# Optimization experiments

Measured on AMD Instinct MI355X. Metric: run time of the kernel, lower is better.

The kernel has to match this reference:

```python
import jax, jax.numpy as jnp
import numpy as np

B, T, C = 2, 2048, 1024
H, D = 16, 64


def setup_inputs() -> dict:
    key = jax.random.key(0)
    ks = jax.random.split(key, 5)
    s = 1.0 / np.sqrt(C)  # keep projections well-scaled
    return {
        "x": jax.random.normal(ks[0], (B, T, C), dtype=jnp.float32),
        "wq": jax.random.normal(ks[1], (C, C), dtype=jnp.float32) * s,
        "wk": jax.random.normal(ks[2], (C, C), dtype=jnp.float32) * s,
        "wv": jax.random.normal(ks[3], (C, C), dtype=jnp.float32) * s,
        "wo": jax.random.normal(ks[4], (C, C), dtype=jnp.float32) * s,
    }


def reference(x, wq, wk, wv, wo):
    # nn.Linear(d,d,bias=False): y = x @ W.T ; weights stored [out,in]
    q = (x @ wq.T).reshape(B, T, H, D).transpose(0, 2, 1, 3)  # [B,H,T,D]
    k = (x @ wk.T).reshape(B, T, H, D).transpose(0, 2, 1, 3)
    v = (x @ wv.T).reshape(B, T, H, D).transpose(0, 2, 1, 3)
    scale = jnp.sqrt(jnp.float32(D))
    scores = jnp.einsum("bhtd,bhsd->bhts", q, k) / scale  # [B,H,T,T]
    # additive causal mask: -inf above the diagonal
    causal = jnp.tril(jnp.ones((T, T), dtype=bool))
    scores = jnp.where(causal[None, None], scores, jnp.float32(-1e9))
    weights = jax.nn.softmax(scores, axis=-1)
    out = jnp.einsum("bhts,bhsd->bhtd", weights, v)  # [B,H,T,D]
    out = out.transpose(0, 2, 1, 3).reshape(B, T, C)
    return out @ wo.T
```

## Files before the change

### kernel.cpp

```cpp
#include <hip/hip_runtime.h>
#include <stdint.h>

#define B_ 2
#define T_ 2048
#define C_ 1024
#define H_ 16
#define D_ 64
#define M_ (B_*T_)

typedef __attribute__((ext_vector_type(8))) short bf16x8;
typedef __attribute__((ext_vector_type(4))) short bf16x4;
typedef __attribute__((ext_vector_type(4))) float f32x4;
typedef unsigned short u16;

#define MFMA32(a, b, c) __builtin_amdgcn_mfma_f32_16x16x32_bf16((a), (b), (c), 0, 0, 0)

__device__ __forceinline__ u16 f2bf(float f) {
  union { float f; uint32_t u; } v; v.f = f;
  uint32_t u = v.u;
  return (u16)((u + 0x7fffu + ((u >> 16) & 1u)) >> 16);
}

__device__ __forceinline__ float exp2_fast(float x) { return __builtin_amdgcn_exp2f(x); }

typedef const __attribute__((address_space(1))) void* gas_t;
typedef __attribute__((address_space(3))) void* las_t;
__device__ __forceinline__ void gld_lds16(const void* g, void* l) {
  __builtin_amdgcn_global_load_lds((gas_t)g, (las_t)l, 16, 0, 0);
}

__global__ void cvt_bf16(const float* __restrict__ src, u16* __restrict__ dst) {
  int i = (blockIdx.x * blockDim.x + threadIdx.x) * 4;
  float4 v = *(const float4*)(src + i);
  ushort4 o;
  o.x = f2bf(v.x); o.y = f2bf(v.y); o.z = f2bf(v.z); o.w = f2bf(v.w);
  *(ushort4*)(dst + i) = o;
}

__global__ void cvt_bf16_w4(const float* __restrict__ s0, const float* __restrict__ s1,
                            const float* __restrict__ s2, const float* __restrict__ s3,
                            u16* __restrict__ d0, u16* __restrict__ d1,
                            u16* __restrict__ d2, u16* __restrict__ d3) {
  const float* s; u16* d;
  switch (blockIdx.y) {
    case 0: s = s0; d = d0; break;
    case 1: s = s1; d = d1; break;
    case 2: s = s2; d = d2; break;
    default: s = s3; d = d3; break;
  }
  int i = (blockIdx.x * blockDim.x + threadIdx.x) * 4;
  float4 v = *(const float4*)(s + i);
  ushort4 o;
  o.x = f2bf(v.x); o.y = f2bf(v.y); o.z = f2bf(v.z); o.w = f2bf(v.w);
  *(ushort4*)(d + i) = o;
}

__device__ __forceinline__ void gemm_core(const u16* __restrict__ A,
                                          const u16* __restrict__ W,
                                          int m0, int n0, int Kt,
                                          f32x4 acc[4][4])
{
  __shared__ u16 As[128*64];
  __shared__ u16 Bs[128*64];
  const int t = threadIdx.x;
  const int lane = t & 63;
  const int wave = t >> 6;
  const int q = lane >> 4;
  const int l15 = lane & 15;
  const int wm = (wave >> 1) * 64;
  const int wn = (wave & 1) * 64;

  #pragma unroll
  for (int i = 0; i < 4; ++i)
    #pragma unroll
    for (int j = 0; j < 4; ++j)
      acc[i][j] = (f32x4){0.f, 0.f, 0.f, 0.f};

  for (int k0 = 0; k0 < Kt; k0 += 64) {
    #pragma unroll
    for (int r = 0; r < 4; ++r) {
      int Lc = r * 256 + t;
      int row = Lc >> 3;
      int gcc = (Lc & 7) ^ (row & 7);
      gld_lds16(A + (size_t)(m0 + row) * Kt + k0 + gcc * 8, As + Lc * 8);
    }
    #pragma unroll
    for (int r = 0; r < 4; ++r) {
      int Lc = r * 256 + t;
      int row = Lc >> 3;
      int gcc = (Lc & 7) ^ (row & 7);
      gld_lds16(W + (size_t)(n0 + row) * Kt + k0 + gcc * 8, Bs + Lc * 8);
    }
    __syncthreads();

    #pragma unroll
    for (int kk = 0; kk < 2; ++kk) {
      bf16x8 af[4], bfr[4];
      #pragma unroll
      for (int i = 0; i < 4; ++i) {
        int m = wm + i * 16 + l15;
        int ch = (kk * 4 + q) ^ (m & 7);
        af[i] = *(const bf16x8*)(As + m * 64 + ch * 8);
      }
      #pragma unroll
      for (int j = 0; j < 4; ++j) {
        int n = wn + j * 16 + l15;
        int ch = (kk * 4 + q) ^ (n & 7);
        bfr[j] = *(const bf16x8*)(Bs + n * 64 + ch * 8);
      }
      #pragma unroll
      for (int i = 0; i < 4; ++i)
        #pragma unroll
        for (int j = 0; j < 4; ++j)
          acc[i][j] = MFMA32(af[i], bfr[j], acc[i][j]);
    }
    __syncthreads();
  }
}

#define QSCALE 0.1803368801111244f
__global__ __launch_bounds__(256, 3)
void gemm_qkv(const u16* __restrict__ X,
              const u16* __restrict__ Wq, const u16* __restrict__ Wk,
              const u16* __restrict__ Wv,
              u16* __restrict__ Q, u16* __restrict__ K, u16* __restrict__ Vt)
{
  const int bm = blockIdx.x;
  const int bn = blockIdx.y;
  const int seg = bn >> 3;
  const int n0 = (bn & 7) * 128;
  const u16* W = (seg == 0) ? Wq : ((seg == 1) ? Wk : Wv);

  f32x4 acc[4][4];
  gemm_core(X, W, bm * 128, n0, C_, acc);

  const int t = threadIdx.x, lane = t & 63, wave = t >> 6;
  const int q = lane >> 4, l15 = lane & 15;
  const int wm = (wave >> 1) * 64, wn = (wave & 1) * 64;
  const float scale = (seg == 0) ? QSCALE : 1.0f;

  #pragma unroll
  for (int i = 0; i < 4; ++i) {
    #pragma unroll
    for (int j = 0; j < 4; ++j) {
      const int mbase = bm * 128 + wm + i * 16 + q * 4;
      const int n = n0 + wn + j * 16 + l15;
      const int h = n >> 6, d = n & 63;
      if (seg < 2) {
        u16* dst = (seg == 0) ? Q : K;
        #pragma unroll
        for (int r = 0; r < 4; ++r) {
          const int m = mbase + r;
          const int b = m >> 11, tt = m & (T_ - 1);
          size_t idx = (((size_t)(b * H_ + h)) * T_ + tt) * D_ + d;
          dst[idx] = f2bf(acc[i][j][r] * scale);
        }
      } else {
        const int b = mbase >> 11, tt = mbase & (T_ - 1);
        const int ttp = (tt & ~31) | ((tt & 12) << 1) | ((tt & 16) >> 2);
        size_t idx = (((size_t)(b * H_ + h)) * D_ + d) * T_ + ttp;
        ushort4 pk;
        pk.x = f2bf(acc[i][j][0]); pk.y = f2bf(acc[i][j][1]);
        pk.z = f2bf(acc[i][j][2]); pk.w = f2bf(acc[i][j][3]);
        *(ushort4*)(Vt + idx) = pk;
      }
    }
  }
}

__global__ __launch_bounds__(256, 2)
void attn(const u16* __restrict__ Q, const u16* __restrict__ K,
          const u16* __restrict__ Vt, u16* __restrict__ Att)
{
  __shared__ u16 Ks[2][64 * 64];
  __shared__ u16 Vs[2][64 * 64];
  const int t = threadIdx.x;
  const int lane = t & 63, wave = t >> 6;
  const int q = lane >> 4, l15 = lane & 15;
  const int pr = blockIdx.x;
  const int bh = blockIdx.y;
  const int qbA = pr * 64;
  const int qbB = (31 - pr) * 64;
  const u16* Qp = Q + (size_t)bh * T_ * D_;
  const u16* Kp = K + (size_t)bh * T_ * D_;
  const u16* Vp = Vt + (size_t)bh * D_ * T_;

  const int rowA = qbA + 4 * l15 + wave;
  const int rowB = qbB + 4 * l15 + wave;
  const u16* qra = Qp + (size_t)rowA * 64;
  const u16* qrb = Qp + (size_t)rowB * 64;
  const bf16x8 aqA0 = *(const bf16x8*)(qra + q * 8);
  const bf16x8 aqA1 = *(const bf16x8*)(qra + 32 + q * 8);
  const bf16x8 aqB0 = *(const bf16x8*)(qrb + q * 8);
  const bf16x8 aqB1 = *(const bf16x8*)(qrb + 32 + q * 8);

  f32x4 oA[4], oB[4];
  #pragma unroll
  for (int j = 0; j < 4; ++j) {
    oA[j] = (f32x4){0.f, 0.f, 0.f, 0.f};
    oB[j] = (f32x4){0.f, 0.f, 0.f, 0.f};
  }
  float lsA = 0.f, lsB = 0.f;

  auto stage = [&](int kb, int buf) {
    #pragma unroll
    for (int r = 0; r < 2; ++r) {
      int c = r * 256 + t, row = c >> 3, gcc = (c & 7) ^ (row & 7);
      gld_lds16(Kp + (size_t)(kb + row) * 64 + gcc * 8, &Ks[buf][c * 8]);
    }
    #pragma unroll
    for (int r = 0; r < 2; ++r) {
      int c = r * 256 + t, row = c >> 3, gcc = (c & 7) ^ (row & 7);
      gld_lds16(Vp + (size_t)row * T_ + kb + gcc * 8, &Vs[buf][c * 8]);
    }
  };

  stage(0, 0);
  int cur = 0;
  for (int kb = 0; kb <= qbB; kb += 64, cur ^= 1) {
    __syncthreads();
    if (kb + 64 <= qbB) stage(kb + 64, cur ^ 1);
    const u16* Kc = &Ks[cur][0];
    const u16* Vc = &Vs[cur][0];

    bf16x8 kf0[4], kf1[4];
    #pragma unroll
    for (int j2 = 0; j2 < 4; ++j2) {
      const int row = j2 * 16 + l15;
      kf0[j2] = *(const bf16x8*)(Kc + row * 64 + ((q)     ^ (row & 7)) * 8);
      kf1[j2] = *(const bf16x8*)(Kc + row * 64 + ((4 + q) ^ (row & 7)) * 8);
    }
    bf16x8 vfrag[4][2];
    #pragma unroll
    for (int j = 0; j < 4; ++j) {
      const int row = j * 16 + l15;
      #pragma unroll
      for (int kk = 0; kk < 2; ++kk) {
        const int ch = (kk * 4 + q) ^ (row & 7);
        vfrag[j][kk] = *(const bf16x8*)(Vc + row * 64 + ch * 8);
      }
    }

    auto tile_compute = [&](const bf16x8 a0, const bf16x8 a1, f32x4* o,
                            float& lsum, int rowg, bool diag) {
      bf16x4 pb[4];
      #pragma unroll
      for (int j2 = 0; j2 < 4; ++j2) {
        f32x4 z = (f32x4){0.f, 0.f, 0.f, 0.f};
        z = MFMA32(kf0[j2], a0, z);
        z = MFMA32(kf1[j2], a1, z);
        if (diag) {
          #pragma unroll
          for (int r = 0; r < 4; ++r) {
            const int key = kb + j2 * 16 + q * 4 + r;
            if (key > rowg) z[r] = -1e30f;
          }
        }
        float p0 = exp2_fast(z[0]), p1 = exp2_fast(z[1]);
        float p2 = exp2_fast(z[2]), p3 = exp2_fast(z[3]);
        lsum += (p0 + p1) + (p2 + p3);
        pb[j2] = (bf16x4){(short)f2bf(p0), (short)f2bf(p1),
                          (short)f2bf(p2), (short)f2bf(p3)};
      }
      #pragma unroll
      for (int kk = 0; kk < 2; ++kk) {
        const bf16x8 pc = __builtin_shufflevector(pb[2 * kk], pb[2 * kk + 1],
                                                  0, 1, 2, 3, 4, 5, 6, 7);
        #pragma unroll
        for (int j = 0; j < 4; ++j)
          o[j] = MFMA32(vfrag[j][kk], pc, o[j]);
      }
    };

    tile_compute(aqB0, aqB1, oB, lsB, rowB, kb == qbB);
    if (kb <= qbA)
      tile_compute(aqA0, aqA1, oA, lsA, rowA, kb == qbA);
  }

  lsA += __shfl_xor(lsA, 16, 64); lsA += __shfl_xor(lsA, 32, 64);
  lsB += __shfl_xor(lsB, 16, 64); lsB += __shfl_xor(lsB, 32, 64);
  const float invA = __builtin_amdgcn_rcpf(lsA);
  const float invB = __builtin_amdgcn_rcpf(lsB);

  const int b = bh >> 4, h = bh & 15;
  #pragma unroll
  for (int j = 0; j < 4; ++j) {
    ushort4 pa, pbk;
    pa.x = f2bf(oA[j][0] * invA); pa.y = f2bf(oA[j][1] * invA);
    pa.z = f2bf(oA[j][2] * invA); pa.w = f2bf(oA[j][3] * invA);
    pbk.x = f2bf(oB[j][0] * invB); pbk.y = f2bf(oB[j][1] * invB);
    pbk.z = f2bf(oB[j][2] * invB); pbk.w = f2bf(oB[j][3] * invB);
    *(ushort4*)(Att + ((size_t)b * T_ + rowA) * C_ + h * 64 + j * 16 + q * 4) = pa;
    *(ushort4*)(Att + ((size_t)b * T_ + rowB) * C_ + h * 64 + j * 16 + q * 4) = pbk;
  }
}

__global__ __launch_bounds__(256, 2)
void gemm_out(const u16* __restrict__ Att, const u16* __restrict__ Wo,
              float* __restrict__ Out)
{
  __shared__ u16 As[64 * 64];
  __shared__ u16 Bs[128 * 64];
  const int t = threadIdx.x;
  const int lane = t & 63, wave = t >> 6;
  const int q = lane >> 4, l15 = lane & 15;
  const int wm = (wave >> 1) * 32, wn = (wave & 1) * 64;
  const int m0 = blockIdx.x * 64, n0 = blockIdx.y * 128;

  f32x4 acc[2][4];
  #pragma unroll
  for (int i = 0; i < 2; ++i)
    #pragma unroll
    for (int j = 0; j < 4; ++j)
      acc[i][j] = (f32x4){0.f, 0.f, 0.f, 0.f};

  for (int k0 = 0; k0 < C_; k0 += 64) {
    #pragma unroll
    for (int r = 0; r < 2; ++r) {
      int Lc = r * 256 + t, row = Lc >> 3, gcc = (Lc & 7) ^ (row & 7);
      gld_lds16(Att + (size_t)(m0 + row) * C_ + k0 + gcc * 8, As + Lc * 8);
    }
    #pragma unroll
    for (int r = 0; r < 4; ++r) {
      int Lc = r * 256 + t, row = Lc >> 3, gcc = (Lc & 7) ^ (row & 7);
      gld_lds16(Wo + (size_t)(n0 + row) * C_ + k0 + gcc * 8, Bs + Lc * 8);
    }
    __syncthreads();

    #pragma unroll
    for (int kk = 0; kk < 2; ++kk) {
      bf16x8 af[2], bfr[4];
      #pragma unroll
      for (int i = 0; i < 2; ++i) {
        int m = wm + i * 16 + l15;
        int ch = (kk * 4 + q) ^ (m & 7);
        af[i] = *(const bf16x8*)(As + m * 64 + ch * 8);
      }
      #pragma unroll
      for (int j = 0; j < 4; ++j) {
        int n = wn + j * 16 + l15;
        int ch = (kk * 4 + q) ^ (n & 7);
        bfr[j] = *(const bf16x8*)(Bs + n * 64 + ch * 8);
      }
      #pragma unroll
      for (int i = 0; i < 2; ++i)
        #pragma unroll
        for (int j = 0; j < 4; ++j)
          acc[i][j] = MFMA32(af[i], bfr[j], acc[i][j]);
    }
    __syncthreads();
  }

  #pragma unroll
  for (int i = 0; i < 2; ++i) {
    #pragma unroll
    for (int j = 0; j < 4; ++j) {
      const int mm = m0 + wm + i * 16 + q * 4;
      const int n = n0 + wn + j * 16 + l15;
      #pragma unroll
      for (int r = 0; r < 4; ++r)
        Out[(size_t)(mm + r) * C_ + n] = acc[i][j][r];
    }
  }
}

extern "C" void kernel_launch(void* const* d_in, const int* in_sizes, int n_in,
                              void* d_out, int out_size, void* d_ws, size_t ws_size,
                              hipStream_t stream) {
  const float* x  = (const float*)d_in[0];
  const float* wq = (const float*)d_in[1];
  const float* wk = (const float*)d_in[2];
  const float* wv = (const float*)d_in[3];
  const float* wo = (const float*)d_in[4];
  float* out = (float*)d_out;

  u16* ws  = (u16*)d_ws;
  u16* xb  = ws;
  u16* wqb = xb  + (size_t)M_ * C_;
  u16* wkb = wqb + (size_t)C_ * C_;
  u16* wvb = wkb + (size_t)C_ * C_;
  u16* wob = wvb + (size_t)C_ * C_;
  u16* Qb  = wob + (size_t)C_ * C_;
  u16* Kb  = Qb  + (size_t)M_ * C_;
  u16* Vtb = Kb  + (size_t)M_ * C_;
  u16* Atb = Vtb + (size_t)M_ * C_;

  cvt_bf16<<<dim3(M_ * C_ / 1024), 256, 0, stream>>>(x, xb);
  cvt_bf16_w4<<<dim3(C_ * C_ / 1024, 4), 256, 0, stream>>>(wq, wk, wv, wo,
                                                           wqb, wkb, wvb, wob);

  gemm_qkv<<<dim3(M_ / 128, 24), 256, 0, stream>>>(xb, wqb, wkb, wvb, Qb, Kb, Vtb);
  attn<<<dim3(16, B_ * H_), 256, 0, stream>>>(Qb, Kb, Vtb, Atb);
  gemm_out<<<dim3(M_ / 64, C_ / 128), 256, 0, stream>>>(Atb, wob, out);
}
```

Before: 171.8 us.

## Merge conversion kernels, transpose GEMM operands for vector stores, widen attention K/V tiles

New measurement: 171.1 us. No clear change (-0.4%).

```diff
diff --git a/kernel.cpp b/kernel.cpp
--- a/kernel.cpp
+++ b/kernel.cpp
@@ -29,30 +29,31 @@
   __builtin_amdgcn_global_load_lds((gas_t)g, (las_t)l, 16, 0, 0);
 }
 
-__global__ void cvt_bf16(const float* __restrict__ src, u16* __restrict__ dst) {
-  int i = (blockIdx.x * blockDim.x + threadIdx.x) * 4;
-  float4 v = *(const float4*)(src + i);
+__global__ void cvt_all(const float* __restrict__ x,
+                        const float* __restrict__ w0, const float* __restrict__ w1,
+                        const float* __restrict__ w2, const float* __restrict__ w3,
+                        u16* __restrict__ xb,
+                        u16* __restrict__ d0, u16* __restrict__ d1,
+                        u16* __restrict__ d2, u16* __restrict__ d3) {
+  size_t i = ((size_t)blockIdx.x * 256 + threadIdx.x) * 4;
+  const float* s; u16* d; size_t off;
+  const size_t NX = (size_t)M_ * C_;
+  const size_t NW = (size_t)C_ * C_;
+  if (i < NX) { s = x; d = xb; off = i; }
+  else {
+    size_t j = i - NX;
+    int w = (int)(j / NW); off = j - (size_t)w * NW;
+    switch (w) {
+      case 0: s = w0; d = d0; break;
+      case 1: s = w1; d = d1; break;
+      case 2: s = w2; d = d2; break;
+      default: s = w3; d = d3; break;
+    }
+  }
+  float4 v = *(const float4*)(s + off);
   ushort4 o;
   o.x = f2bf(v.x); o.y = f2bf(v.y); o.z = f2bf(v.z); o.w = f2bf(v.w);
-  *(ushort4*)(dst + i) = o;
-}
-
-__global__ void cvt_bf16_w4(const float* __restrict__ s0, const float* __restrict__ s1,
-                            const float* __restrict__ s2, const float* __restrict__ s3,
-                            u16* __restrict__ d0, u16* __restrict__ d1,
-                            u16* __restrict__ d2, u16* __restrict__ d3) {
-  const float* s; u16* d;
-  switch (blockIdx.y) {
-    case 0: s = s0; d = d0; break;
-    case 1: s = s1; d = d1; break;
-    case 2: s = s2; d = d2; break;
-    default: s = s3; d = d3; break;
-  }
-  int i = (blockIdx.x * blockDim.x + threadIdx.x) * 4;
-  float4 v = *(const float4*)(s + i);
-  ushort4 o;
-  o.x = f2bf(v.x); o.y = f2bf(v.y); o.z = f2bf(v.z); o.w = f2bf(v.w);
-  *(ushort4*)(d + i) = o;
+  *(ushort4*)(d + off) = o;
 }
 
 __device__ __forceinline__ void gemm_core(const u16* __restrict__ A,
@@ -128,35 +129,43 @@
   const int bm = blockIdx.x;
   const int bn = blockIdx.y;
   const int seg = bn >> 3;
-  const int n0 = (bn & 7) * 128;
-  const u16* W = (seg == 0) ? Wq : ((seg == 1) ? Wk : Wv);
-
-  f32x4 acc[4][4];
-  gemm_core(X, W, bm * 128, n0, C_, acc);
+  const int nb = (bn & 7) * 128;
 
   const int t = threadIdx.x, lane = t & 63, wave = t >> 6;
   const int q = lane >> 4, l15 = lane & 15;
   const int wm = (wave >> 1) * 64, wn = (wave & 1) * 64;
-  const float scale = (seg == 0) ? QSCALE : 1.0f;
-
-  #pragma unroll
-  for (int i = 0; i < 4; ++i) {
-    #pragma unroll
-    for (int j = 0; j < 4; ++j) {
-      const int mbase = bm * 128 + wm + i * 16 + q * 4;
-      const int n = n0 + wn + j * 16 + l15;
-      const int h = n >> 6, d = n & 63;
-      if (seg < 2) {
-        u16* dst = (seg == 0) ? Q : K;
-        #pragma unroll
-        for (int r = 0; r < 4; ++r) {
-          const int m = mbase + r;
-          const int b = m >> 11, tt = m & (T_ - 1);
-          size_t idx = (((size_t)(b * H_ + h)) * T_ + tt) * D_ + d;
-          dst[idx] = f2bf(acc[i][j][r] * scale);
-        }
-      } else {
+
+  f32x4 acc[4][4];
+
+  if (seg < 2) {
+    const u16* W = (seg == 0) ? Wq : Wk;
+    gemm_core(W, X, nb, bm * 128, C_, acc);
+    u16* dst = (seg == 0) ? Q : K;
+    const float scale = (seg == 0) ? QSCALE : 1.0f;
+    #pragma unroll
+    for (int i = 0; i < 4; ++i) {
+      #pragma unroll
+      for (int j = 0; j < 4; ++j) {
+        const int o = nb + wm + i * 16 + q * 4;
+        const int h = o >> 6, d = o & 63;
+        const int mtok = bm * 128 + wn + j * 16 + l15;
+        const int b = mtok >> 11, tt = mtok & (T_ - 1);
+        ushort4 pk;
+        pk.x = f2bf(acc[i][j][0] * scale); pk.y = f2bf(acc[i][j][1] * scale);
+        pk.z = f2bf(acc[i][j][2] * scale); pk.w = f2bf(acc[i][j][3] * scale);
+        *(ushort4*)(dst + (((size_t)(b * H_ + h)) * T_ + tt) * D_ + d) = pk;
+      }
+    }
+  } else {
+    gemm_core(X, Wv, bm * 128, nb, C_, acc);
+    #pragma unroll
+    for (int i = 0; i < 4; ++i) {
+      #pragma unroll
+      for (int j = 0; j < 4; ++j) {
+        const int mbase = bm * 128 + wm + i * 16 + q * 4;
         const int b = mbase >> 11, tt = mbase & (T_ - 1);
+        const int n = nb + wn + j * 16 + l15;
+        const int h = n >> 6, d = n & 63;
         const int ttp = (tt & ~31) | ((tt & 12) << 1) | ((tt & 16) >> 2);
         size_t idx = (((size_t)(b * H_ + h)) * D_ + d) * T_ + ttp;
         ushort4 pk;
@@ -172,8 +181,8 @@
 void attn(const u16* __restrict__ Q, const u16* __restrict__ K,
           const u16* __restrict__ Vt, u16* __restrict__ Att)
 {
-  __shared__ u16 Ks[2][64 * 64];
-  __shared__ u16 Vs[2][64 * 64];
+  __shared__ u16 Ks[2][128 * 64];
+  __shared__ u16 Vs[2][64 * 128];
   const int t = threadIdx.x;
   const int lane = t & 63, wave = t >> 6;
   const int q = lane >> 4, l15 = lane & 15;
@@ -204,77 +213,83 @@
 
   auto stage = [&](int kb, int buf) {
     #pragma unroll
-    for (int r = 0; r < 2; ++r) {
+    for (int r = 0; r < 4; ++r) {
       int c = r * 256 + t, row = c >> 3, gcc = (c & 7) ^ (row & 7);
       gld_lds16(Kp + (size_t)(kb + row) * 64 + gcc * 8, &Ks[buf][c * 8]);
     }
     #pragma unroll
-    for (int r = 0; r < 2; ++r) {
-      int c = r * 256 + t, row = c >> 3, gcc = (c & 7) ^ (row & 7);
+    for (int r = 0; r < 4; ++r) {
+      int c = r * 256 + t, row = c >> 4, gcc = (c & 15) ^ (row & 15);
       gld_lds16(Vp + (size_t)row * T_ + kb + gcc * 8, &Vs[buf][c * 8]);
     }
   };
 
   stage(0, 0);
   int cur = 0;
-  for (int kb = 0; kb <= qbB; kb += 64, cur ^= 1) {
+  for (int kb = 0; kb <= qbB; kb += 128, cur ^= 1) {
     __syncthreads();
-    if (kb + 64 <= qbB) stage(kb + 64, cur ^ 1);
+    if (kb + 128 <= qbB) stage(kb + 128, cur ^ 1);
     const u16* Kc = &Ks[cur][0];
     const u16* Vc = &Vs[cur][0];
 
-    bf16x8 kf0[4], kf1[4];
-    #pragma unroll
-    for (int j2 = 0; j2 < 4; ++j2) {
-      const int row = j2 * 16 + l15;
-      kf0[j2] = *(const bf16x8*)(Kc + row * 64 + ((q)     ^ (row & 7)) * 8);
-      kf1[j2] = *(const bf16x8*)(Kc + row * 64 + ((4 + q) ^ (row & 7)) * 8);
-    }
-    bf16x8 vfrag[4][2];
-    #pragma unroll
-    for (int j = 0; j < 4; ++j) {
-      const int row = j * 16 + l15;
-      #pragma unroll
-      for (int kk = 0; kk < 2; ++kk) {
-        const int ch = (kk * 4 + q) ^ (row & 7);
-        vfrag[j][kk] = *(const bf16x8*)(Vc + row * 64 + ch * 8);
-      }
-    }
-
-    auto tile_compute = [&](const bf16x8 a0, const bf16x8 a1, f32x4* o,
-                            float& lsum, int rowg, bool diag) {
-      bf16x4 pb[4];
+    #pragma unroll
+    for (int s = 0; s < 2; ++s) {
+      const int kbase = kb + s * 64;
+      if (kbase > qbB) break;
+
+      bf16x8 kf0[4], kf1[4];
       #pragma unroll
       for (int j2 = 0; j2 < 4; ++j2) {
-        f32x4 z = (f32x4){0.f, 0.f, 0.f, 0.f};
-        z = MFMA32(kf0[j2], a0, z);
-        z = MFMA32(kf1[j2], a1, z);
-        if (diag) {
+        const int rw = s * 64 + j2 * 16 + l15;
+        kf0[j2] = *(const bf16x8*)(Kc + rw * 64 + ((q)     ^ (rw & 7)) * 8);
+        kf1[j2] = *(const bf16x8*)(Kc + rw * 64 + ((4 + q) ^ (rw & 7)) * 8);
+      }
+      bf16x8 vfrag[4][2];
+      #pragma unroll
+      for (int j = 0; j < 4; ++j) {
+        const int rw = j * 16 + l15;
+        #pragma unroll
+        for (int kk = 0; kk < 2; ++kk) {
+          const int cc = ((2 * s + kk) * 4 + q) ^ (rw & 15);
+          vfrag[j][kk] = *(const bf16x8*)(Vc + rw * 128 + cc * 8);
+        }
+      }
+
+      auto tile_compute = [&](const bf16x8 a0, const bf16x8 a1, f32x4* o,
+                              float& lsum, int rowg, bool diag) {
+        bf16x4 pb[4];
+        #pragma unroll
+        for (int j2 = 0; j2 < 4; ++j2) {
+          f32x4 z = (f32x4){0.f, 0.f, 0.f, 0.f};
+          z = MFMA32(kf0[j2], a0, z);
+          z = MFMA32(kf1[j2], a1, z);
+          if (diag) {
+            #pragma unroll
+            for (int r = 0; r < 4; ++r) {
+              const int key = kbase + j2 * 16 + q * 4 + r;
+              if (key > rowg) z[r] = -1e30f;
+            }
+          }
+          float p0 = exp2_fast(z[0]), p1 = exp2_fast(z[1]);
+          float p2 = exp2_fast(z[2]), p3 = exp2_fast(z[3]);
+          lsum += (p0 + p1) + (p2 + p3);
+          pb[j2] = (bf16x4){(short)f2bf(p0), (short)f2bf(p1),
+                            (short)f2bf(p2), (short)f2bf(p3)};
+        }
+        #pragma unroll
+        for (int kk = 0; kk < 2; ++kk) {
+          const bf16x8 pc = __builtin_shufflevector(pb[2 * kk], pb[2 * kk + 1],
+                                                    0, 1, 2, 3, 4, 5, 6, 7);
           #pragma unroll
-          for (int r = 0; r < 4; ++r) {
-            const int key = kb + j2 * 16 + q * 4 + r;
-            if (key > rowg) z[r] = -1e30f;
-          }
+          for (int j = 0; j < 4; ++j)
+            o[j] = MFMA32(vfrag[j][kk], pc, o[j]);
         }
-        float p0 = exp2_fast(z[0]), p1 = exp2_fast(z[1]);
-        float p2 = exp2_fast(z[2]), p3 = exp2_fast(z[3]);
-        lsum += (p0 + p1) + (p2 + p3);
-        pb[j2] = (bf16x4){(short)f2bf(p0), (short)f2bf(p1),
-                          (short)f2bf(p2), (short)f2bf(p3)};
-      }
-      #pragma unroll
-      for (int kk = 0; kk < 2; ++kk) {
-        const bf16x8 pc = __builtin_shufflevector(pb[2 * kk], pb[2 * kk + 1],
-                                                  0, 1, 2, 3, 4, 5, 6, 7);
-        #pragma unroll
-        for (int j = 0; j < 4; ++j)
-          o[j] = MFMA32(vfrag[j][kk], pc, o[j]);
-      }
-    };
-
-    tile_compute(aqB0, aqB1, oB, lsB, rowB, kb == qbB);
-    if (kb <= qbA)
-      tile_compute(aqA0, aqA1, oA, lsA, rowA, kb == qbA);
+      };
+
+      tile_compute(aqB0, aqB1, oB, lsB, rowB, kbase == qbB);
+      if (kbase <= qbA)
+        tile_compute(aqA0, aqA1, oA, lsA, rowA, kbase == qbA);
+    }
   }
 
   lsA += __shfl_xor(lsA, 16, 64); lsA += __shfl_xor(lsA, 32, 64);
@@ -305,7 +320,8 @@
   const int lane = t & 63, wave = t >> 6;
   const int q = lane >> 4, l15 = lane & 15;
   const int wm = (wave >> 1) * 32, wn = (wave & 1) * 64;
-  const int m0 = blockIdx.x * 64, n0 = blockIdx.y * 128;
+  const int m0 = blockIdx.x * 64;
+  const int n0 = blockIdx.y * 128;
 
   f32x4 acc[2][4];
   #pragma unroll
@@ -318,12 +334,12 @@
     #pragma unroll
     for (int r = 0; r < 2; ++r) {
       int Lc = r * 256 + t, row = Lc >> 3, gcc = (Lc & 7) ^ (row & 7);
-      gld_lds16(Att + (size_t)(m0 + row) * C_ + k0 + gcc * 8, As + Lc * 8);
+      gld_lds16(Wo + (size_t)(m0 + row) * C_ + k0 + gcc * 8, As + Lc * 8);
     }
     #pragma unroll
     for (int r = 0; r < 4; ++r) {
       int Lc = r * 256 + t, row = Lc >> 3, gcc = (Lc & 7) ^ (row & 7);
-      gld_lds16(Wo + (size_t)(n0 + row) * C_ + k0 + gcc * 8, Bs + Lc * 8);
+      gld_lds16(Att + (size_t)(n0 + row) * C_ + k0 + gcc * 8, Bs + Lc * 8);
     }
     __syncthreads();
 
@@ -355,11 +371,10 @@
   for (int i = 0; i < 2; ++i) {
     #pragma unroll
     for (int j = 0; j < 4; ++j) {
-      const int mm = m0 + wm + i * 16 + q * 4;
-      const int n = n0 + wn + j * 16 + l15;
-      #pragma unroll
-      for (int r = 0; r < 4; ++r)
-        Out[(size_t)(mm + r) * C_ + n] = acc[i][j][r];
+      const int o = m0 + wm + i * 16 + q * 4;
+      const int tok = n0 + wn + j * 16 + l15;
+      float4 st = {acc[i][j][0], acc[i][j][1], acc[i][j][2], acc[i][j][3]};
+      *(float4*)(Out + (size_t)tok * C_ + o) = st;
     }
   }
 }
@@ -385,11 +400,10 @@
   u16* Vtb = Kb  + (size_t)M_ * C_;
   u16* Atb = Vtb + (size_t)M_ * C_;
 
-  cvt_bf16<<<dim3(M_ * C_ / 1024), 256, 0, stream>>>(x, xb);
-  cvt_bf16_w4<<<dim3(C_ * C_ / 1024, 4), 256, 0, stream>>>(wq, wk, wv, wo,
-                                                           wqb, wkb, wvb, wob);
+  cvt_all<<<dim3((M_ * C_ + 4 * C_ * C_) / 1024), 256, 0, stream>>>(
+      x, wq, wk, wv, wo, xb, wqb, wkb, wvb, wob);
 
   gemm_qkv<<<dim3(M_ / 128, 24), 256, 0, stream>>>(xb, wqb, wkb, wvb, Qb, Kb, Vtb);
   attn<<<dim3(16, B_ * H_), 256, 0, stream>>>(Qb, Kb, Vtb, Atb);
-  gemm_out<<<dim3(M_ / 64, C_ / 128), 256, 0, stream>>>(Atb, wob, out);
-}
+  gemm_out<<<dim3(C_ / 64, M_ / 128), 256, 0, stream>>>(Atb, wob, out);
+}
```
